# Kernel optimization log

Measured on AMD Instinct MI355X. Metric: run time of the kernel, lower is better.

Reference implementation:

```python
import jax, jax.numpy as jnp
import numpy as np

# Fixed production-scale sizes (equal-sized graphs so unbatch == reshape)
B, NQ, ND = 64, 32, 512     # graph pairs, query nodes/graph, data nodes/graph
DIN, D, K = 64, 128, 16     # GCN_in_size, GCN_out_size, NTN_k
DEG = 8                     # average degree


def _gcn(x, src, dst, W, b):
    """GCNConv with self loops + symmetric normalization (PyG semantics)."""
    N = x.shape[0]
    loop = jnp.arange(N)
    s = jnp.concatenate([src, loop])
    t = jnp.concatenate([dst, loop])
    deg = jax.ops.segment_sum(jnp.ones_like(t, x.dtype), t, num_segments=N)
    dinv = jnp.where(deg > 0, deg ** -0.5, 0.0)
    norm = (dinv[s] * dinv[t])[:, None]
    h = x @ W
    return jax.ops.segment_sum(h[s] * norm, t, num_segments=N) + b


def _three_gcn(x, ei, W1, b1, W2, b2, W3, b3):
    src, dst = ei[0], ei[1]
    h1 = jax.nn.relu(_gcn(x, src, dst, W1, b1))
    h2 = jax.nn.relu(_gcn(h1, src, dst, W2, b2))
    h3 = jax.nn.relu(_gcn(h2, src, dst, W3, b3))
    return h1, h2, h3


def _level(q, d, Wn, Vn, bn, cw, cb):
    """att_layer + NTN + elementwise mult + 1x1 conv + softmax over data nodes.
    q: [B,NQ,D], d: [B,ND,D] -> (softmaxed map [B,NQ,ND], raw map, he [B,K,NQ,ND])."""
    att = jax.nn.softmax(jnp.einsum('bqd,bnd->bqn', q, d) / jnp.sqrt(jnp.float32(D)), axis=-1)
    qW = jnp.einsum('bqd,kde->bkqe', q, Wn)           # [B,K,NQ,D]
    bil = jnp.einsum('bkqe,bne->bkqn', qW, d)          # [B,K,NQ,ND]
    lq = jnp.einsum('kd,bqd->bkq', Vn[:, :D], q)[:, :, :, None]
    ld = jnp.einsum('kd,bnd->bkn', Vn[:, D:], d)[:, :, None, :]
    he = jax.nn.sigmoid(bil + lq + ld + bn[None, :, None, None]) * att[:, None]
    e_raw = jnp.einsum('k,bkqn->bqn', cw, he) + cb     # 1x1 Conv2d(K->1)
    return jax.nn.softmax(e_raw, axis=-1), e_raw, he


def reference(x_d, edge_index_d, x_q, edge_index_q, batch_index_d, batch_index_q,
              W1, b1, W2, b2, W3, b3,
              Wn1, Vn1, bn1, cw1, cb1,
              Wn2, Vn2, bn2, cw2, cb2,
              Wn3, Vn3, bn3, cw3, cb3,
              w_end, b_end):
    d1, d2, d3 = _three_gcn(x_d, edge_index_d, W1, b1, W2, b2, W3, b3)
    q1, q2, q3 = _three_gcn(x_q, edge_index_q, W1, b1, W2, b2, W3, b3)
    # unbatch: batch indices are sorted with equal graph sizes -> reshape
    d1, d2, d3 = (t.reshape(B, ND, D) for t in (d1, d2, d3))
    q1, q2, q3 = (t.reshape(B, NQ, D) for t in (q1, q2, q3))
    e1, _, he1 = _level(q1, d1, Wn1, Vn1, bn1, cw1, cb1)
    _, e2raw, he2 = _level(q2, d2, Wn2, Vn2, bn2, cw2, cb2)
    e3, _, he3 = _level(q3, d3, Wn3, Vn3, bn3, cw3, cb3)
    # Faithful to source quirks: the zip unpack `e1,e2,e3,h1,h2,h1` rebinds h1 to
    # he_3 (he_1 is never used, he_3 appears twice) and end2 enters the concat
    # PRE-softmax (the softmaxed version was assigned to unused `nd2`).
    stack = jnp.concatenate([e1[:, None], e2raw[:, None], e3[:, None], he3, he2, he3], axis=1)
    out = jnp.einsum('c,bcqn->bqn', w_end, stack) + b_end  # con_end 1x1 conv + squeeze
    return jax.nn.softmax(out, axis=-1)                    # softmax over data nodes


def setup_inputs() -> dict:
    key = jax.random.key(0)
    k = jax.random.split(key, 40)
    n = jax.random.normal
    Nd, Nq = B * ND, B * NQ
    Ed, Eq = Nd * DEG, Nq * DEG
    gid_d = jnp.repeat(jnp.arange(B), ND * DEG)
    gid_q = jnp.repeat(jnp.arange(B), NQ * DEG)
    inp = {
        'x_d': n(k[0], (Nd, DIN), jnp.float32),
        'x_q': n(k[1], (Nq, DIN), jnp.float32),
        'edge_index_d': jnp.stack([jax.random.randint(k[2], (Ed,), 0, ND) + gid_d * ND,
                                   jax.random.randint(k[3], (Ed,), 0, ND) + gid_d * ND]),
        'edge_index_q': jnp.stack([jax.random.randint(k[4], (Eq,), 0, NQ) + gid_q * NQ,
                                   jax.random.randint(k[5], (Eq,), 0, NQ) + gid_q * NQ]),
        'batch_index_d': jnp.repeat(jnp.arange(B), ND),
        'batch_index_q': jnp.repeat(jnp.arange(B), NQ),
        'W1': n(k[6], (DIN, D), jnp.float32) / np.sqrt(DIN), 'b1': jnp.zeros((D,), jnp.float32),
        'W2': n(k[7], (D, D), jnp.float32) / np.sqrt(D), 'b2': jnp.zeros((D,), jnp.float32),
        'W3': n(k[8], (D, D), jnp.float32) / np.sqrt(D), 'b3': jnp.zeros((D,), jnp.float32),
    }
    for i, l in enumerate(('1', '2', '3')):
        inp['Wn' + l] = n(k[10 + 4 * i], (K, D, D), jnp.float32) / np.sqrt(D)
        inp['Vn' + l] = n(k[11 + 4 * i], (K, 2 * D), jnp.float32) / np.sqrt(2 * D)
        inp['bn' + l] = jnp.zeros((K,), jnp.float32)
        inp['cw' + l] = n(k[12 + 4 * i], (K,), jnp.float32) / np.sqrt(K)
        inp['cb' + l] = jnp.zeros((1,), jnp.float32)
    inp['w_end'] = n(k[25], (3 * K + 3,), jnp.float32) / np.sqrt(3 * K + 3)
    inp['b_end'] = jnp.zeros((1,), jnp.float32)
    return inp
```

## Files before the change

### kernel.cpp

```cpp
#include <hip/hip_runtime.h>
#include <math.h>

namespace {
constexpr int cB  = 64;
constexpr int cNQ = 32;
constexpr int cND = 512;
constexpr int cNd = cB * cND;
constexpr int cNq = cB * cNQ;
constexpr int cEd = cNd * 8;
constexpr int cEq = cNq * 8;
constexpr int LD_STRIDE = 516;
constexpr int NB_CVT = 2188, NB_T2BF = 808, NB_CNT = (cEd + cEq) / 256;
constexpr int NB_FILL = (cEd + cEq) / 256;
}

#define F4C(p) (*(const float4*)(p))
#define F4W(p) (*(float4*)(p))

typedef __attribute__((ext_vector_type(8))) __bf16 bf16x8;
typedef __attribute__((ext_vector_type(4))) float floatx4;

__device__ __forceinline__ ushort f2bf(float f) {
  union { float f; unsigned u; } v;
  v.f = f;
  unsigned u = v.u;
  return (ushort)((u + 0x7fffu + ((u >> 16) & 1u)) >> 16);
}
__device__ __forceinline__ float bf2f(ushort u) {
  union { unsigned u; float f; } v;
  v.u = ((unsigned)u) << 16;
  return v.f;
}
__device__ __forceinline__ float4 us4f4(ushort4 u) {
  return make_float4(bf2f(u.x), bf2f(u.y), bf2f(u.z), bf2f(u.w));
}
__device__ __forceinline__ ushort4 f4us4(float4 f) {
  ushort4 o;
  o.x = f2bf(f.x); o.y = f2bf(f.y); o.z = f2bf(f.z); o.w = f2bf(f.w);
  return o;
}
__device__ __forceinline__ float fexp2(float x) {
#if __has_builtin(__builtin_amdgcn_exp2f)
  return __builtin_amdgcn_exp2f(x);
#else
  return exp2f(x);
#endif
}
__device__ __forceinline__ float frcp(float x) {
#if __has_builtin(__builtin_amdgcn_rcpf)
  return __builtin_amdgcn_rcpf(x);
#else
  return 1.0f / x;
#endif
}
__device__ __forceinline__ float fsigmoid(float z) {
  return frcp(1.0f + fexp2(z * -1.4426950408889634f));
}
__device__ __forceinline__ float fexp(float x) { return fexp2(x * 1.4426950408889634f); }

__device__ __forceinline__ int swz_g(int j) { return (((j >> 3) & 7) << 3) | (j & 7); }

__global__ __launch_bounds__(256) void k_front(
    const float* __restrict__ xd, const float* __restrict__ xq,
    const float* __restrict__ v0, const float* __restrict__ v1,
    const float* __restrict__ v2, ushort* __restrict__ oxd, ushort* __restrict__ oxq,
    ushort* __restrict__ ov0, ushort* __restrict__ ov1, ushort* __restrict__ ov2,
    const float* __restrict__ W1, const float* __restrict__ W2,
    const float* __restrict__ W3, const float* __restrict__ Wn0,
    const float* __restrict__ Wn1, const float* __restrict__ Wn2,
    ushort* __restrict__ o1, ushort* __restrict__ o2, ushort* __restrict__ o3,
    ushort* __restrict__ on0, ushort* __restrict__ on1, ushort* __restrict__ on2,
    const int* __restrict__ dst_d, const int* __restrict__ dst_q,
    int* __restrict__ cnt_d, int* __restrict__ cnt_q) {
  __shared__ float tile[32][33];
  int blk = blockIdx.x, tid = threadIdx.x;
  if (blk < NB_CVT) {
    const float* src;
    ushort* dst;
    int i;
    if (blk < 2048) { src = xd; dst = oxd; i = blk * 256 + tid; }
    else if (blk < 2176) { src = xq; dst = oxq; i = (blk - 2048) * 256 + tid; }
    else if (blk < 2180) { src = v0; dst = ov0; i = (blk - 2176) * 256 + tid; }
    else if (blk < 2184) { src = v1; dst = ov1; i = (blk - 2180) * 256 + tid; }
    else { src = v2; dst = ov2; i = (blk - 2184) * 256 + tid; }
    *(ushort4*)(dst + (size_t)i * 4) = f4us4(F4C(src + (size_t)i * 4));
  } else if (blk < NB_CVT + NB_T2BF) {
    int b5 = blk - NB_CVT;
    const float* in;
    ushort* out;
    int R, C, bt, t;
    if (b5 < 8)        { in = W1;  out = o1;  R = 64;  C = 128; bt = 0; t = b5; }
    else if (b5 < 24)  { in = W2;  out = o2;  R = 128; C = 128; bt = 0; t = b5 - 8; }
    else if (b5 < 40)  { in = W3;  out = o3;  R = 128; C = 128; bt = 0; t = b5 - 24; }
    else if (b5 < 296) { in = Wn0; out = on0; R = 128; C = 128; bt = (b5 - 40) >> 4;  t = (b5 - 40) & 15; }
    else if (b5 < 552) { in = Wn1; out = on1; R = 128; C = 128; bt = (b5 - 296) >> 4; t = (b5 - 296) & 15; }
    else               { in = Wn2; out = on2; R = 128; C = 128; bt = (b5 - 552) >> 4; t = (b5 - 552) & 15; }
    int tilesC = C >> 5;
    int tr = t / tilesC, tc = t - tr * tilesC;
    int tx = tid & 31, ty = tid >> 5;
    const float* ib = in + (size_t)bt * R * C;
    ushort* ob = out + (size_t)bt * R * C;
#pragma unroll
    for (int i = 0; i < 4; ++i)
      tile[ty + i * 8][tx] = ib[(tr * 32 + ty + i * 8) * C + tc * 32 + tx];
    __syncthreads();
#pragma unroll
    for (int i = 0; i < 4; ++i)
      ob[(size_t)(tc * 32 + ty + i * 8) * R + tr * 32 + tx] = f2bf(tile[tx][ty + i * 8]);
  } else {
    int i = (blk - NB_CVT - NB_T2BF) * 256 + tid;
    if (i < cEd) atomicAdd(&cnt_d[dst_d[i]], 1);
    else atomicAdd(&cnt_q[dst_q[i - cEd]], 1);
  }
}

__global__ __launch_bounds__(512) void k_scan_dinv(
    const int* __restrict__ cnt_d, const int* __restrict__ cnt_q,
    int* __restrict__ rp_d, int* __restrict__ rp_q,
    float* __restrict__ dinv_d, float* __restrict__ dinv_q) {
  __shared__ int sh[512];
  int blk = blockIdx.x, tid = threadIdx.x;
  if (blk < 64) {
    int v = cnt_d[blk * 512 + tid];
    sh[tid] = v;
    __syncthreads();
    for (int off = 1; off < 512; off <<= 1) {
      int t = (tid >= off) ? sh[tid - off] : 0;
      __syncthreads();
      sh[tid] += t;
      __syncthreads();
    }
    rp_d[blk * 512 + tid] = blk * 4096 + sh[tid] - v;
  } else if (blk < 68) {
    int g = (blk - 64) * 16 + (tid >> 5);
    int lane32 = tid & 31;
    int v = cnt_q[g * 32 + lane32];
    int incl = v;
#pragma unroll
    for (int off = 1; off < 32; off <<= 1) {
      int t = __shfl_up(incl, off, 32);
      if (lane32 >= off) incl += t;
    }
    rp_q[g * 32 + lane32] = g * 256 + incl - v;
  } else {
    int i = (blk - 68) * 512 + tid;
    if (i < cNd) dinv_d[i] = 1.0f / sqrtf((float)(cnt_d[i] + 1));
    else dinv_q[i - cNd] = 1.0f / sqrtf((float)(cnt_q[i - cNd] + 1));
  }
}

__global__ __launch_bounds__(256) void k_fill_gemm1(
    const int* __restrict__ src_d, const int* __restrict__ dst_d,
    const int* __restrict__ src_q, const int* __restrict__ dst_q,
    const int* __restrict__ rp_d, const int* __restrict__ rp_q,
    int* __restrict__ cur_d, int* __restrict__ cur_q, int* __restrict__ col_d,
    int* __restrict__ col_q, const ushort* __restrict__ xdbf,
    const ushort* __restrict__ xqbf, const ushort* __restrict__ w1T,
    const float* __restrict__ dinv_d, const float* __restrict__ dinv_q,
    ushort* __restrict__ htmp) {
  int blk = blockIdx.x, tid = threadIdx.x;
  if (blk < NB_FILL) {
    int i = blk * 256 + tid;
    if (i < cEd) {
      int d = dst_d[i];
      int p = atomicAdd(&cur_d[d], 1);
      col_d[rp_d[d] + p] = src_d[i];
    } else {
      int j = i - cEd;
      int d = dst_q[j];
      int p = atomicAdd(&cur_q[d], 1);
      col_q[rp_q[d] + p] = src_q[j];
    }
    return;
  }
  int blk2 = blk - NB_FILL;
  int wave = tid >> 6, lane = tid & 63;
  int col = lane & 15, quad = lane >> 4;
  bool isQ = blk2 >= 512;
  int node0;
  if (isQ) node0 = (blk2 - 512) * 64;
  else node0 = swz_g(blk2) * 512 + (blk2 >> 6) * 64;
  int mloc = node0 + wave * 16;
  const ushort* X = isQ ? xqbf : xdbf;
  const float* dv = isQ ? dinv_q : dinv_d;
  size_t hbase = isQ ? (size_t)cNd : 0;
  floatx4 acc[8];
#pragma unroll
  for (int ct = 0; ct < 8; ++ct)
#pragma unroll
    for (int r = 0; r < 4; ++r) acc[ct][r] = 0.0f;
#pragma unroll
  for (int kc = 0; kc < 2; ++kc) {
    bf16x8 a = *(const bf16x8*)(X + (size_t)(mloc + col) * 64 + kc * 32 + quad * 8);
#pragma unroll
    for (int ct = 0; ct < 8; ++ct) {
      bf16x8 b = *(const bf16x8*)(w1T + (size_t)(ct * 16 + col) * 64 + kc * 32 + quad * 8);
      acc[ct] = __builtin_amdgcn_mfma_f32_16x16x32_bf16(a, b, acc[ct], 0, 0, 0);
    }
  }
  float sc[4];
#pragma unroll
  for (int r = 0; r < 4; ++r) sc[r] = dv[mloc + quad * 4 + r];
#pragma unroll
  for (int ct = 0; ct < 8; ++ct)
#pragma unroll
    for (int r = 0; r < 4; ++r)
      htmp[(hbase + mloc + quad * 4 + r) * 128 + ct * 16 + col] = f2bf(acc[ct][r] * sc[r]);
}

__global__ __launch_bounds__(256) void gmn_gather_merged(
    const ushort* __restrict__ htmp, const int* __restrict__ rp_d,
    const int* __restrict__ cnt_d, const int* __restrict__ col_d,
    const float* __restrict__ dinv_d, const int* __restrict__ rp_q,
    const int* __restrict__ cnt_q, const int* __restrict__ col_q,
    const float* __restrict__ dinv_q, const float* __restrict__ bias,
    ushort* __restrict__ dbf, ushort* __restrict__ qbf) {
  int blk = blockIdx.x, tid = threadIdx.x;
  bool isQ = blk >= 4096;
  int node;
  if (isQ) {
    int j = blk - 4096;
    node = swz_g(j) * 32 + (j >> 6) * 8 + (tid >> 5);
  } else {
    node = swz_g(blk) * 512 + (blk >> 6) * 8 + (tid >> 5);
  }
  int l = tid & 31;
  const ushort* hs = htmp + (isQ ? (size_t)cNd * 128 : 0);
  const int* rp = isQ ? rp_q : rp_d;
  const int* cnt = isQ ? cnt_q : cnt_d;
  const int* col = isQ ? col_q : col_d;
  const float* dinv = isQ ? dinv_q : dinv_d;
  ushort* outp = isQ ? qbf : dbf;
  int c = cnt[node], s0 = rp[node];
  float dt = dinv[node];
  float4 acc = us4f4(*(const ushort4*)(hs + (size_t)node * 128 + l * 4));
  int cm = c < 32 ? c : 32;
  for (int j0 = 0; j0 < cm; j0 += 8) {
    int ss[8];
    ushort4 v[8];
#pragma unroll
    for (int t = 0; t < 8; ++t) {
      int jj = j0 + t;
      ss[t] = (jj < cm) ? col[s0 + jj] : -1;
    }
#pragma unroll
    for (int t = 0; t < 8; ++t)
      if (ss[t] >= 0) v[t] = *(const ushort4*)(hs + (size_t)ss[t] * 128 + l * 4);
#pragma unroll
    for (int t = 0; t < 8; ++t) {
      if (ss[t] >= 0) {
        float4 f = us4f4(v[t]);
        acc.x += f.x; acc.y += f.y; acc.z += f.z; acc.w += f.w;
      }
    }
  }
  for (int j = 32; j < c; ++j) {
    int s = col[s0 + j];
    float4 f = us4f4(*(const ushort4*)(hs + (size_t)s * 128 + l * 4));
    acc.x += f.x; acc.y += f.y; acc.z += f.z; acc.w += f.w;
  }
  float4 bv = F4C(bias + l * 4);
  float4 r;
  r.x = fmaxf(acc.x * dt + bv.x, 0.0f);
  r.y = fmaxf(acc.y * dt + bv.y, 0.0f);
  r.z = fmaxf(acc.z * dt + bv.z, 0.0f);
  r.w = fmaxf(acc.w * dt + bv.w, 0.0f);
  *(ushort4*)(outp + (size_t)node * 128 + l * 4) = f4us4(r);
}

__global__ __launch_bounds__(256) void gmn_qw(const ushort* __restrict__ qbf,
                                              const ushort* __restrict__ wnT,
                                              ushort* __restrict__ qw) {
  int blk = blockIdx.x, tid = threadIdx.x;
  int wave = tid >> 6, lane = tid & 63;
  int col = lane & 15, quad = lane >> 4;
  int b = swz_g(blk), k = blk >> 6;
  int et0 = wave * 2;
  floatx4 acc[2][2];
#pragma unroll
  for (int qt = 0; qt < 2; ++qt)
#pragma unroll
    for (int ei = 0; ei < 2; ++ei)
#pragma unroll
      for (int r = 0; r < 4; ++r) acc[qt][ei][r] = 0.0f;
#pragma unroll
  for (int kc = 0; kc < 4; ++kc) {
    bf16x8 a0 = *(const bf16x8*)(qbf + (size_t)(b * 32 + col) * 128 + kc * 32 + quad * 8);
    bf16x8 a1 = *(const bf16x8*)(qbf + (size_t)(b * 32 + 16 + col) * 128 + kc * 32 + quad * 8);
#pragma unroll
    for (int ei = 0; ei < 2; ++ei) {
      bf16x8 bf = *(const bf16x8*)(wnT + (size_t)(k * 128 + (et0 + ei) * 16 + col) * 128 +
                                   kc * 32 + quad * 8);
      acc[0][ei] = __builtin_amdgcn_mfma_f32_16x16x32_bf16(a0, bf, acc[0][ei], 0, 0, 0);
      acc[1][ei] = __builtin_amdgcn_mfma_f32_16x16x32_bf16(a1, bf, acc[1][ei], 0, 0, 0);
    }
  }
#pragma unroll
  for (int qt = 0; qt < 2; ++qt)
#pragma unroll
    for (int ei = 0; ei < 2; ++ei)
#pragma unroll
      for (int r = 0; r < 4; ++r)
        qw[((size_t)(b * 16 + k) << 12) + (qt * 16 + quad * 4 + r) * 128 +
           (et0 + ei) * 16 + col] = f2bf(acc[qt][ei][r]);
}

__global__ __launch_bounds__(512, 2) void k_level_gemm(
    const ushort* __restrict__ qbf, const ushort* __restrict__ dbf,
    const ushort* __restrict__ qw, const ushort* __restrict__ vnbf,
    const float* __restrict__ bn, const float* __restrict__ cw,
    const float* __restrict__ w_end, const float* __restrict__ b_end,
    int o1, int o2, int hasF, int do_sm, int mode, int widx,
    float* __restrict__ accb, float* __restrict__ out,
    const ushort* __restrict__ gWT, const float* __restrict__ dinv_d,
    const float* __restrict__ dinv_q, ushort* __restrict__ htmp) {
  __shared__ float s_ld[16 * LD_STRIDE];
  __shared__ float s_lq[16 * 16];
  __shared__ float s_red[16 * 8];
  int tid = threadIdx.x;
  int wave = tid >> 6, lane = tid & 63;
  int col = lane & 15, quad = lane >> 4;

  if (blockIdx.x >= 128) {
    int gblk = blockIdx.x - 128;
    bool isQ = gblk >= 256;
    int node0;
    if (isQ) node0 = (gblk - 256) * 128;
    else node0 = swz_g(gblk) * 512 + (gblk >> 6) * 128;
    int mloc = node0 + wave * 16;
    const ushort* X = isQ ? qbf : dbf;
    const float* dv = isQ ? dinv_q : dinv_d;
    size_t hbase = isQ ? (size_t)cNd : 0;
    floatx4 acc[8];
#pragma unroll
    for (int ct = 0; ct < 8; ++ct)
#pragma unroll
      for (int r = 0; r < 4; ++r) acc[ct][r] = 0.0f;
#pragma unroll
    for (int kc = 0; kc < 4; ++kc) {
      bf16x8 a = *(const bf16x8*)(X + (size_t)(mloc + col) * 128 + kc * 32 + quad * 8);
#pragma unroll
      for (int ct = 0; ct < 8; ++ct) {
        bf16x8 b = *(const bf16x8*)(gWT + (size_t)(ct * 16 + col) * 128 + kc * 32 + quad * 8);
        acc[ct] = __builtin_amdgcn_mfma_f32_16x16x32_bf16(a, b, acc[ct], 0, 0, 0);
      }
    }
    float sc[4];
#pragma unroll
    for (int r = 0; r < 4; ++r) sc[r] = dv[mloc + quad * 4 + r];
#pragma unroll
    for (int ct = 0; ct < 8; ++ct)
#pragma unroll
      for (int r = 0; r < 4; ++r)
        htmp[(hbase + mloc + quad * 4 + r) * 128 + ct * 16 + col] = f2bf(acc[ct][r] * sc[r]);
    return;
  }

  int b = swz_g(blockIdx.x & 63);
  int qh = blockIdx.x >> 6;
  int n0 = wave * 64;

  bf16x8 bfr[4][4];
#pragma unroll
  for (int s = 0; s < 4; ++s)
#pragma unroll
    for (int kc = 0; kc < 4; ++kc)
      bfr[s][kc] = *(const bf16x8*)(dbf + ((size_t)(b * 512 + n0 + s * 16 + col) << 7) +
                                    kc * 32 + quad * 8);
  bf16x8 aq[4];
#pragma unroll
  for (int kc = 0; kc < 4; ++kc)
    aq[kc] = *(const bf16x8*)(qbf + (size_t)(b * 32 + qh * 16 + col) * 128 +
                              kc * 32 + quad * 8);

  floatx4 att[4];
#pragma unroll
  for (int s = 0; s < 4; ++s)
#pragma unroll
    for (int r = 0; r < 4; ++r) att[s][r] = 0.0f;
#pragma unroll
  for (int kc = 0; kc < 4; ++kc)
#pragma unroll
    for (int s = 0; s < 4; ++s)
      att[s] = __builtin_amdgcn_mfma_f32_16x16x32_bf16(aq[kc], bfr[s][kc], att[s], 0, 0, 0);
  const float sc = 0.088388347648318440550f;
#pragma unroll
  for (int s = 0; s < 4; ++s)
#pragma unroll
    for (int r = 0; r < 4; ++r) att[s][r] *= sc;

  {
    bf16x8 vn2[4];
#pragma unroll
    for (int kc = 0; kc < 4; ++kc)
      vn2[kc] = *(const bf16x8*)(vnbf + col * 256 + 128 + kc * 32 + quad * 8);
#pragma unroll
    for (int s = 0; s < 4; ++s) {
      floatx4 lda;
#pragma unroll
      for (int r = 0; r < 4; ++r) lda[r] = 0.0f;
#pragma unroll
      for (int kc = 0; kc < 4; ++kc)
        lda = __builtin_amdgcn_mfma_f32_16x16x32_bf16(bfr[s][kc], vn2[kc], lda, 0, 0, 0);
#pragma unroll
      for (int r = 0; r < 4; ++r)
        s_ld[col * LD_STRIDE + n0 + s * 16 + quad * 4 + r] = lda[r];
    }
  }
  if (wave == 0) {
    bf16x8 vn1[4];
#pragma unroll
    for (int kc = 0; kc < 4; ++kc)
      vn1[kc] = *(const bf16x8*)(vnbf + col * 256 + kc * 32 + quad * 8);
    floatx4 lqa;
#pragma unroll
    for (int r = 0; r < 4; ++r) lqa[r] = 0.0f;
#pragma unroll
    for (int kc = 0; kc < 4; ++kc)
      lqa = __builtin_amdgcn_mfma_f32_16x16x32_bf16(aq[kc], vn1[kc], lqa, 0, 0, 0);
#pragma unroll
    for (int r = 0; r < 4; ++r) s_lq[col * 16 + quad * 4 + r] = lqa[r];
  }
  __syncthreads();

  float red[4], M[4];
#pragma unroll
  for (int r = 0; r < 4; ++r) {
    float m = fmaxf(fmaxf(att[0][r], att[1][r]), fmaxf(att[2][r], att[3][r]));
#pragma unroll
    for (int o = 1; o < 16; o <<= 1) m = fmaxf(m, __shfl_xor(m, o, 64));
    red[r] = m;
  }
  if (col == 0)
#pragma unroll
    for (int r = 0; r < 4; ++r) s_red[(quad * 4 + r) * 8 + wave] = red[r];
  __syncthreads();
#pragma unroll
  for (int r = 0; r < 4; ++r) {
    float m = s_red[(quad * 4 + r) * 8];
#pragma unroll
    for (int w = 1; w < 8; ++w) m = fmaxf(m, s_red[(quad * 4 + r) * 8 + w]);
    M[r] = m;
  }
  __syncthreads();
#pragma unroll
  for (int s = 0; s < 4; ++s)
#pragma unroll
    for (int r = 0; r < 4; ++r) att[s][r] = fexp(att[s][r] - M[r]);
#pragma unroll
  for (int r = 0; r < 4; ++r) {
    float m = att[0][r] + att[1][r] + att[2][r] + att[3][r];
#pragma unroll
    for (int o = 1; o < 16; o <<= 1) m += __shfl_xor(m, o, 64);
    red[r] = m;
  }
  if (col == 0)
#pragma unroll
    for (int r = 0; r < 4; ++r) s_red[(quad * 4 + r) * 8 + wave] = red[r];
  __syncthreads();
#pragma unroll
  for (int r = 0; r < 4; ++r) {
    float m = s_red[(quad * 4 + r) * 8];
#pragma unroll
    for (int w = 1; w < 8; ++w) m += s_red[(quad * 4 + r) * 8 + w];
    M[r] = frcp(m);
  }
  __syncthreads();
#pragma unroll
  for (int s = 0; s < 4; ++s)
#pragma unroll
    for (int r = 0; r < 4; ++r) att[s][r] *= M[r];

  floatx4 eacc[4], facc[4];
#pragma unroll
  for (int s = 0; s < 4; ++s)
#pragma unroll
    for (int r = 0; r < 4; ++r) { eacc[s][r] = 0.0f; facc[s][r] = 0.0f; }

#pragma unroll 4
  for (int k = 0; k < 16; ++k) {
    const ushort* qk = qw + ((size_t)(b * 16 + k) << 12) + (qh * 16 + col) * 128 + quad * 8;
    bf16x8 a0 = *(const bf16x8*)(qk);
    bf16x8 a1 = *(const bf16x8*)(qk + 32);
    bf16x8 a2 = *(const bf16x8*)(qk + 64);
    bf16x8 a3 = *(const bf16x8*)(qk + 96);
    floatx4 bil[4];
#pragma unroll
    for (int s = 0; s < 4; ++s) {
#pragma unroll
      for (int r = 0; r < 4; ++r) bil[s][r] = 0.0f;
      bil[s] = __builtin_amdgcn_mfma_f32_16x16x32_bf16(a0, bfr[s][0], bil[s], 0, 0, 0);
      bil[s] = __builtin_amdgcn_mfma_f32_16x16x32_bf16(a1, bfr[s][1], bil[s], 0, 0, 0);
      bil[s] = __builtin_amdgcn_mfma_f32_16x16x32_bf16(a2, bfr[s][2], bil[s], 0, 0, 0);
      bil[s] = __builtin_amdgcn_mfma_f32_16x16x32_bf16(a3, bfr[s][3], bil[s], 0, 0, 0);
    }
    float bnk = bn[k], cwk = cw[k];
    float wkk = 0.0f;
    if (hasF) {
      wkk = w_end[o1 + k];
      if (o2 >= 0) wkk += w_end[o2 + k];
    }
    float lqv[4];
#pragma unroll
    for (int r = 0; r < 4; ++r) lqv[r] = s_lq[k * 16 + quad * 4 + r] + bnk;
#pragma unroll
    for (int s = 0; s < 4; ++s) {
      float ldv = s_ld[k * LD_STRIDE + n0 + s * 16 + col];
#pragma unroll
      for (int r = 0; r < 4; ++r) {
        float sg = fsigmoid(bil[s][r] + lqv[r] + ldv);
        eacc[s][r] += cwk * sg;
        facc[s][r] += wkk * sg;
      }
    }
  }

#pragma unroll
  for (int s = 0; s < 4; ++s)
#pragma unroll
    for (int r = 0; r < 4; ++r) {
      eacc[s][r] *= att[s][r];
      facc[s][r] *= att[s][r];
    }
  if (do_sm) {
#pragma unroll
    for (int r = 0; r < 4; ++r) {
      float m = fmaxf(fmaxf(eacc[0][r], eacc[1][r]), fmaxf(eacc[2][r], eacc[3][r]));
#pragma unroll
      for (int o = 1; o < 16; o <<= 1) m = fmaxf(m, __shfl_xor(m, o, 64));
      red[r] = m;
    }
    if (col == 0)
#pragma unroll
      for (int r = 0; r < 4; ++r) s_red[(quad * 4 + r) * 8 + wave] = red[r];
    __syncthreads();
#pragma unroll
    for (int r = 0; r < 4; ++r) {
      float m = s_red[(quad * 4 + r) * 8];
#pragma unroll
      for (int w = 1; w < 8; ++w) m = fmaxf(m, s_red[(quad * 4 + r) * 8 + w]);
      M[r] = m;
    }
    __syncthreads();
#pragma unroll
    for (int s = 0; s < 4; ++s)
#pragma unroll
      for (int r = 0; r < 4; ++r) eacc[s][r] = fexp(eacc[s][r] - M[r]);
#pragma unroll
    for (int r = 0; r < 4; ++r) {
      float m = eacc[0][r] + eacc[1][r] + eacc[2][r] + eacc[3][r];
#pragma unroll
      for (int o = 1; o < 16; o <<= 1) m += __shfl_xor(m, o, 64);
      red[r] = m;
    }
    if (col == 0)
#pragma unroll
      for (int r = 0; r < 4; ++r) s_red[(quad * 4 + r) * 8 + wave] = red[r];
    __syncthreads();
#pragma unroll
    for (int r = 0; r < 4; ++r) {
      float m = s_red[(quad * 4 + r) * 8];
#pragma unroll
      for (int w = 1; w < 8; ++w) m += s_red[(quad * 4 + r) * 8 + w];
      M[r] = frcp(m);
    }
    __syncthreads();
#pragma unroll
    for (int s = 0; s < 4; ++s)
#pragma unroll
      for (int r = 0; r < 4; ++r) eacc[s][r] *= M[r];
  }
  float w = w_end[widx];
#pragma unroll
  for (int s = 0; s < 4; ++s)
#pragma unroll
    for (int r = 0; r < 4; ++r) eacc[s][r] = w * eacc[s][r] + (hasF ? facc[s][r] : 0.0f);

  if (mode == 0) {
#pragma unroll
    for (int s = 0; s < 4; ++s)
#pragma unroll
      for (int r = 0; r < 4; ++r)
        accb[((size_t)(b * 32 + qh * 16 + quad * 4 + r) << 9) + n0 + s * 16 + col] =
            eacc[s][r];
  } else if (mode == 1) {
#pragma unroll
    for (int s = 0; s < 4; ++s)
#pragma unroll
      for (int r = 0; r < 4; ++r)
        accb[((size_t)(b * 32 + qh * 16 + quad * 4 + r) << 9) + n0 + s * 16 + col] +=
            eacc[s][r];
  } else {
    float be = b_end[0];
#pragma unroll
    for (int s = 0; s < 4; ++s)
#pragma unroll
      for (int r = 0; r < 4; ++r)
        eacc[s][r] += accb[((size_t)(b * 32 + qh * 16 + quad * 4 + r) << 9) +
                           n0 + s * 16 + col] + be;
#pragma unroll
    for (int r = 0; r < 4; ++r) {
      float m = fmaxf(fmaxf(eacc[0][r], eacc[1][r]), fmaxf(eacc[2][r], eacc[3][r]));
#pragma unroll
      for (int o = 1; o < 16; o <<= 1) m = fmaxf(m, __shfl_xor(m, o, 64));
      red[r] = m;
    }
    if (col == 0)
#pragma unroll
      for (int r = 0; r < 4; ++r) s_red[(quad * 4 + r) * 8 + wave] = red[r];
    __syncthreads();
#pragma unroll
    for (int r = 0; r < 4; ++r) {
      float m = s_red[(quad * 4 + r) * 8];
#pragma unroll
      for (int w2 = 1; w2 < 8; ++w2) m = fmaxf(m, s_red[(quad * 4 + r) * 8 + w2]);
      M[r] = m;
    }
    __syncthreads();
#pragma unroll
    for (int s = 0; s < 4; ++s)
#pragma unroll
      for (int r = 0; r < 4; ++r) eacc[s][r] = fexp(eacc[s][r] - M[r]);
#pragma unroll
    for (int r = 0; r < 4; ++r) {
      float m = eacc[0][r] + eacc[1][r] + eacc[2][r] + eacc[3][r];
#pragma unroll
      for (int o = 1; o < 16; o <<= 1) m += __shfl_xor(m, o, 64);
      red[r] = m;
    }
    if (col == 0)
#pragma unroll
      for (int r = 0; r < 4; ++r) s_red[(quad * 4 + r) * 8 + wave] = red[r];
    __syncthreads();
#pragma unroll
    for (int r = 0; r < 4; ++r) {
      float m = s_red[(quad * 4 + r) * 8];
#pragma unroll
      for (int w2 = 1; w2 < 8; ++w2) m += s_red[(quad * 4 + r) * 8 + w2];
      M[r] = frcp(m);
    }
#pragma unroll
    for (int s = 0; s < 4; ++s)
#pragma unroll
      for (int r = 0; r < 4; ++r)
        out[((size_t)(b * 32 + qh * 16 + quad * 4 + r) << 9) + n0 + s * 16 + col] =
            eacc[s][r] * M[r];
  }
}

extern "C" void kernel_launch(void* const* d_in, const int* in_sizes, int n_in,
                              void* d_out, int out_size, void* d_ws, size_t ws_size,
                              hipStream_t stream) {
  (void)in_sizes; (void)n_in; (void)out_size; (void)ws_size;
  const float* x_d = (const float*)d_in[0];
  const float* x_q = (const float*)d_in[1];
  const int* ei_d = (const int*)d_in[2];
  const int* ei_q = (const int*)d_in[3];
  const float* W1 = (const float*)d_in[6];
  const float* b1 = (const float*)d_in[7];
  const float* W2 = (const float*)d_in[8];
  const float* b2 = (const float*)d_in[9];
  const float* W3 = (const float*)d_in[10];
  const float* b3 = (const float*)d_in[11];
  const float* Wn[3] = {(const float*)d_in[12], (const float*)d_in[17], (const float*)d_in[22]};
  const float* Vn[3] = {(const float*)d_in[13], (const float*)d_in[18], (const float*)d_in[23]};
  const float* bn[3] = {(const float*)d_in[14], (const float*)d_in[19], (const float*)d_in[24]};
  const float* cw[3] = {(const float*)d_in[15], (const float*)d_in[20], (const float*)d_in[25]};
  const float* w_end = (const float*)d_in[27];
  const float* b_end = (const float*)d_in[28];
  float* out = (float*)d_out;

  char* wsp = (char*)d_ws;
  auto alloc = [&](size_t nbytes) {
    void* p = (void*)wsp;
    wsp += (nbytes + 255) & ~(size_t)255;
    return p;
  };
  int* cnt_d = (int*)alloc(cNd * 4);
  int* cnt_q = (int*)alloc(cNq * 4);
  int* cur_d = (int*)alloc(cNd * 4);
  int* cur_q = (int*)alloc(cNq * 4);
  float* dinv_d = (float*)alloc(cNd * 4);
  float* dinv_q = (float*)alloc(cNq * 4);
  int* rp_d = (int*)alloc(cNd * 4);
  int* rp_q = (int*)alloc(cNq * 4);
  int* col_d = (int*)alloc((size_t)cEd * 4);
  int* col_q = (int*)alloc((size_t)cEq * 4);
  ushort* xdbf = (ushort*)alloc((size_t)cNd * 64 * 2);
  ushort* xqbf = (ushort*)alloc((size_t)cNq * 64 * 2);
  ushort* w1T = (ushort*)alloc(128 * 64 * 2);
  ushort* w2T = (ushort*)alloc(128 * 128 * 2);
  ushort* w3T = (ushort*)alloc(128 * 128 * 2);
  ushort* wnT[3];
  for (int l = 0; l < 3; ++l) wnT[l] = (ushort*)alloc((size_t)16 * 128 * 128 * 2);
  ushort* vnbf[3];
  for (int l = 0; l < 3; ++l) vnbf[l] = (ushort*)alloc(16 * 256 * 2);
  ushort* htmp = (ushort*)alloc((size_t)(cNd + cNq) * 128 * 2);
  ushort* dbf = (ushort*)alloc((size_t)cNd * 128 * 2);
  ushort* qbf[3];
  for (int l = 0; l < 3; ++l) qbf[l] = (ushort*)alloc((size_t)cNq * 128 * 2);
  float* accb = (float*)alloc((size_t)cB * cNQ * cND * 4);
  ushort* qwbuf = (ushort*)alloc((size_t)cB * 16 * 32 * 128 * 2);

  const int* src_d = ei_d;
  const int* dst_d = ei_d + cEd;
  const int* src_q = ei_q;
  const int* dst_q = ei_q + cEq;

  hipMemsetAsync(cnt_d, 0, (size_t)2 * (cNd + cNq) * 4, stream);

  k_front<<<NB_CVT + NB_T2BF + NB_CNT, 256, 0, stream>>>(
      x_d, x_q, Vn[0], Vn[1], Vn[2], xdbf, xqbf, vnbf[0], vnbf[1], vnbf[2], W1, W2,
      W3, Wn[0], Wn[1], Wn[2], w1T, w2T, w3T, wnT[0], wnT[1], wnT[2], dst_d, dst_q,
      cnt_d, cnt_q);

  k_scan_dinv<<<136, 512, 0, stream>>>(cnt_d, cnt_q, rp_d, rp_q, dinv_d, dinv_q);

  k_fill_gemm1<<<NB_FILL + 544, 256, 0, stream>>>(
      src_d, dst_d, src_q, dst_q, rp_d, rp_q, cur_d, cur_q, col_d, col_q, xdbf, xqbf,
      w1T, dinv_d, dinv_q, htmp);

  const float* bias[3] = {b1, b2, b3};
  const ushort* nextWT[3] = {w2T, w3T, nullptr};
  const int o1s[3] = {0, 19, 3};
  const int o2s[3] = {-1, -1, 35};
  const int hasF[3] = {0, 1, 1};
  const int dosms[3] = {1, 0, 1};
  const int modes[3] = {0, 1, 2};

  for (int l = 0; l < 3; ++l) {
    gmn_gather_merged<<<(cNd + cNq) / 8, 256, 0, stream>>>(
        htmp, rp_d, cnt_d, col_d, dinv_d, rp_q, cnt_q, col_q, dinv_q, bias[l], dbf,
        qbf[l]);
    gmn_qw<<<1024, 256, 0, stream>>>(qbf[l], wnT[l], qwbuf);
    int grid = (l < 2) ? (128 + 272) : 128;
    k_level_gemm<<<grid, 512, 0, stream>>>(
        qbf[l], dbf, qwbuf, vnbf[l], bn[l], cw[l], w_end, b_end, o1s[l], o2s[l],
        hasF[l], dosms[l], modes[l], l, accb, out, nextWT[l], dinv_d, dinv_q, htmp);
  }
}
```

Baseline: 300.6 us.

## Restructure per-level GCN/NTN schedule to shift query-path work into neighboring kernels

Splits the per-level launches into two merged kernels. The first does the data-graph gather, then the query projection qW and the next-level query GEMM. The second does the level GEMM, the next data GEMM, and now also the query gather for the next level. Because the small query-path work runs alongside larger independent work, the schedule drops from nine launches to seven and shortens the serial dependency chain. In exchange, block-index dispatch gets more complex, and blocks of very different cost now share one grid, which can hurt load balance.

```diff
diff --git a/kernel.cpp b/kernel.cpp
--- a/kernel.cpp
+++ b/kernel.cpp
@@ -15,7 +15,6 @@
 }
 
 #define F4C(p) (*(const float4*)(p))
-#define F4W(p) (*(float4*)(p))
 
 typedef __attribute__((ext_vector_type(8))) __bf16 bf16x8;
 typedef __attribute__((ext_vector_type(4))) float floatx4;
@@ -59,6 +58,76 @@
 __device__ __forceinline__ float fexp(float x) { return fexp2(x * 1.4426950408889634f); }
 
 __device__ __forceinline__ int swz_g(int j) { return (((j >> 3) & 7) << 3) | (j & 7); }
+
+__device__ __forceinline__ void dev_gather_node(
+    int node, int l, const ushort* __restrict__ hs, const int* __restrict__ rp,
+    const int* __restrict__ cnt, const int* __restrict__ col,
+    const float* __restrict__ dinv, const float* __restrict__ bias,
+    ushort* __restrict__ outp) {
+  int c = cnt[node], s0 = rp[node];
+  float dt = dinv[node];
+  float4 acc = us4f4(*(const ushort4*)(hs + (size_t)node * 128 + l * 4));
+  int cm = c < 32 ? c : 32;
+  for (int j0 = 0; j0 < cm; j0 += 8) {
+    int ss[8];
+    ushort4 v[8];
+#pragma unroll
+    for (int t = 0; t < 8; ++t) {
+      int jj = j0 + t;
+      ss[t] = (jj < cm) ? col[s0 + jj] : -1;
+    }
+#pragma unroll
+    for (int t = 0; t < 8; ++t)
+      if (ss[t] >= 0) v[t] = *(const ushort4*)(hs + (size_t)ss[t] * 128 + l * 4);
+#pragma unroll
+    for (int t = 0; t < 8; ++t) {
+      if (ss[t] >= 0) {
+        float4 f = us4f4(v[t]);
+        acc.x += f.x; acc.y += f.y; acc.z += f.z; acc.w += f.w;
+      }
+    }
+  }
+  for (int j = 32; j < c; ++j) {
+    int s = col[s0 + j];
+    float4 f = us4f4(*(const ushort4*)(hs + (size_t)s * 128 + l * 4));
+    acc.x += f.x; acc.y += f.y; acc.z += f.z; acc.w += f.w;
+  }
+  float4 bv = F4C(bias + l * 4);
+  float4 r;
+  r.x = fmaxf(acc.x * dt + bv.x, 0.0f);
+  r.y = fmaxf(acc.y * dt + bv.y, 0.0f);
+  r.z = fmaxf(acc.z * dt + bv.z, 0.0f);
+  r.w = fmaxf(acc.w * dt + bv.w, 0.0f);
+  *(ushort4*)(outp + (size_t)node * 128 + l * 4) = f4us4(r);
+}
+
+__device__ __forceinline__ void dev_gemm128(
+    int mloc, const ushort* __restrict__ X, const ushort* __restrict__ WT,
+    const float* __restrict__ dv, ushort* __restrict__ H, size_t hbase,
+    int col, int quad) {
+  floatx4 acc[8];
+#pragma unroll
+  for (int ct = 0; ct < 8; ++ct)
+#pragma unroll
+    for (int r = 0; r < 4; ++r) acc[ct][r] = 0.0f;
+#pragma unroll
+  for (int kc = 0; kc < 4; ++kc) {
+    bf16x8 a = *(const bf16x8*)(X + (size_t)(mloc + col) * 128 + kc * 32 + quad * 8);
+#pragma unroll
+    for (int ct = 0; ct < 8; ++ct) {
+      bf16x8 b = *(const bf16x8*)(WT + (size_t)(ct * 16 + col) * 128 + kc * 32 + quad * 8);
+      acc[ct] = __builtin_amdgcn_mfma_f32_16x16x32_bf16(a, b, acc[ct], 0, 0, 0);
+    }
+  }
+  float sc[4];
+#pragma unroll
+  for (int r = 0; r < 4; ++r) sc[r] = dv[mloc + quad * 4 + r];
+#pragma unroll
+  for (int ct = 0; ct < 8; ++ct)
+#pragma unroll
+    for (int r = 0; r < 4; ++r)
+      H[(hbase + mloc + quad * 4 + r) * 128 + ct * 16 + col] = f2bf(acc[ct][r] * sc[r]);
+}
 
 __global__ __launch_bounds__(256) void k_front(
     const float* __restrict__ xd, const float* __restrict__ xq,
@@ -208,104 +277,74 @@
       htmp[(hbase + mloc + quad * 4 + r) * 128 + ct * 16 + col] = f2bf(acc[ct][r] * sc[r]);
 }
 
-__global__ __launch_bounds__(256) void gmn_gather_merged(
-    const ushort* __restrict__ htmp, const int* __restrict__ rp_d,
+__global__ __launch_bounds__(512, 4) void k_e1(
+    int aux, ushort* __restrict__ htmp, const int* __restrict__ rp_d,
     const int* __restrict__ cnt_d, const int* __restrict__ col_d,
     const float* __restrict__ dinv_d, const int* __restrict__ rp_q,
     const int* __restrict__ cnt_q, const int* __restrict__ col_q,
     const float* __restrict__ dinv_q, const float* __restrict__ bias,
-    ushort* __restrict__ dbf, ushort* __restrict__ qbf) {
-  int blk = blockIdx.x, tid = threadIdx.x;
-  bool isQ = blk >= 4096;
-  int node;
-  if (isQ) {
-    int j = blk - 4096;
-    node = swz_g(j) * 32 + (j >> 6) * 8 + (tid >> 5);
-  } else {
-    node = swz_g(blk) * 512 + (blk >> 6) * 8 + (tid >> 5);
-  }
-  int l = tid & 31;
-  const ushort* hs = htmp + (isQ ? (size_t)cNd * 128 : 0);
-  const int* rp = isQ ? rp_q : rp_d;
-  const int* cnt = isQ ? cnt_q : cnt_d;
-  const int* col = isQ ? col_q : col_d;
-  const float* dinv = isQ ? dinv_q : dinv_d;
-  ushort* outp = isQ ? qbf : dbf;
-  int c = cnt[node], s0 = rp[node];
-  float dt = dinv[node];
-  float4 acc = us4f4(*(const ushort4*)(hs + (size_t)node * 128 + l * 4));
-  int cm = c < 32 ? c : 32;
-  for (int j0 = 0; j0 < cm; j0 += 8) {
-    int ss[8];
-    ushort4 v[8];
-#pragma unroll
-    for (int t = 0; t < 8; ++t) {
-      int jj = j0 + t;
-      ss[t] = (jj < cm) ? col[s0 + jj] : -1;
-    }
-#pragma unroll
-    for (int t = 0; t < 8; ++t)
-      if (ss[t] >= 0) v[t] = *(const ushort4*)(hs + (size_t)ss[t] * 128 + l * 4);
-#pragma unroll
-    for (int t = 0; t < 8; ++t) {
-      if (ss[t] >= 0) {
-        float4 f = us4f4(v[t]);
-        acc.x += f.x; acc.y += f.y; acc.z += f.z; acc.w += f.w;
-      }
-    }
-  }
-  for (int j = 32; j < c; ++j) {
-    int s = col[s0 + j];
-    float4 f = us4f4(*(const ushort4*)(hs + (size_t)s * 128 + l * 4));
-    acc.x += f.x; acc.y += f.y; acc.z += f.z; acc.w += f.w;
-  }
-  float4 bv = F4C(bias + l * 4);
-  float4 r;
-  r.x = fmaxf(acc.x * dt + bv.x, 0.0f);
-  r.y = fmaxf(acc.y * dt + bv.y, 0.0f);
-  r.z = fmaxf(acc.z * dt + bv.z, 0.0f);
-  r.w = fmaxf(acc.w * dt + bv.w, 0.0f);
-  *(ushort4*)(outp + (size_t)node * 128 + l * 4) = f4us4(r);
-}
-
-__global__ __launch_bounds__(256) void gmn_qw(const ushort* __restrict__ qbf,
-                                              const ushort* __restrict__ wnT,
-                                              ushort* __restrict__ qw) {
+    ushort* __restrict__ dbf, ushort* __restrict__ qbf_out,
+    const ushort* __restrict__ qbf_lvl, const ushort* __restrict__ wnT,
+    ushort* __restrict__ qw, const ushort* __restrict__ gWT) {
   int blk = blockIdx.x, tid = threadIdx.x;
   int wave = tid >> 6, lane = tid & 63;
   int col = lane & 15, quad = lane >> 4;
-  int b = swz_g(blk), k = blk >> 6;
-  int et0 = wave * 2;
-  floatx4 acc[2][2];
-#pragma unroll
-  for (int qt = 0; qt < 2; ++qt)
-#pragma unroll
-    for (int ei = 0; ei < 2; ++ei)
-#pragma unroll
-      for (int r = 0; r < 4; ++r) acc[qt][ei][r] = 0.0f;
-#pragma unroll
-  for (int kc = 0; kc < 4; ++kc) {
-    bf16x8 a0 = *(const bf16x8*)(qbf + (size_t)(b * 32 + col) * 128 + kc * 32 + quad * 8);
-    bf16x8 a1 = *(const bf16x8*)(qbf + (size_t)(b * 32 + 16 + col) * 128 + kc * 32 + quad * 8);
-#pragma unroll
-    for (int ei = 0; ei < 2; ++ei) {
-      bf16x8 bf = *(const bf16x8*)(wnT + (size_t)(k * 128 + (et0 + ei) * 16 + col) * 128 +
-                                   kc * 32 + quad * 8);
-      acc[0][ei] = __builtin_amdgcn_mfma_f32_16x16x32_bf16(a0, bf, acc[0][ei], 0, 0, 0);
-      acc[1][ei] = __builtin_amdgcn_mfma_f32_16x16x32_bf16(a1, bf, acc[1][ei], 0, 0, 0);
-    }
-  }
-#pragma unroll
-  for (int qt = 0; qt < 2; ++qt)
-#pragma unroll
-    for (int ei = 0; ei < 2; ++ei)
-#pragma unroll
-      for (int r = 0; r < 4; ++r)
-        qw[((size_t)(b * 16 + k) << 12) + (qt * 16 + quad * 4 + r) * 128 +
-           (et0 + ei) * 16 + col] = f2bf(acc[qt][ei][r]);
-}
-
-__global__ __launch_bounds__(512, 2) void k_level_gemm(
+  int sec, sblk;
+  if (aux == 0) {
+    if (blk < 2048) { sec = 0; sblk = blk; } else { sec = 1; sblk = blk - 2048; }
+  } else if (aux == 1) {
+    if (blk < 2048) { sec = 0; sblk = blk; }
+    else if (blk < 2560) { sec = 2; sblk = blk - 2048; }
+    else { sec = 3; sblk = blk - 2560; }
+  } else {
+    if (blk < 512) { sec = 2; sblk = blk; } else { sec = 3; sblk = blk - 512; }
+  }
+
+  if (sec == 0) {
+    int node = swz_g(sblk & 63) * 512 + (sblk >> 6) * 16 + (tid >> 5);
+    dev_gather_node(node, tid & 31, htmp, rp_d, cnt_d, col_d, dinv_d, bias, dbf);
+  } else if (sec == 1) {
+    int node = swz_g(sblk & 63) * 32 + (sblk >> 6) * 16 + (tid >> 5);
+    dev_gather_node(node, tid & 31, htmp + (size_t)cNd * 128, rp_q, cnt_q, col_q,
+                    dinv_q, bias, qbf_out);
+  } else if (sec == 2) {
+    int b = swz_g(sblk & 63);
+    int k = (sblk >> 6) * 2 + (wave >> 2);
+    int et0 = (wave & 3) * 2;
+    floatx4 acc[2][2];
+#pragma unroll
+    for (int qt = 0; qt < 2; ++qt)
+#pragma unroll
+      for (int ei = 0; ei < 2; ++ei)
+#pragma unroll
+        for (int r = 0; r < 4; ++r) acc[qt][ei][r] = 0.0f;
+#pragma unroll
+    for (int kc = 0; kc < 4; ++kc) {
+      bf16x8 a0 = *(const bf16x8*)(qbf_lvl + (size_t)(b * 32 + col) * 128 + kc * 32 + quad * 8);
+      bf16x8 a1 = *(const bf16x8*)(qbf_lvl + (size_t)(b * 32 + 16 + col) * 128 + kc * 32 + quad * 8);
+#pragma unroll
+      for (int ei = 0; ei < 2; ++ei) {
+        bf16x8 bf = *(const bf16x8*)(wnT + (size_t)(k * 128 + (et0 + ei) * 16 + col) * 128 +
+                                     kc * 32 + quad * 8);
+        acc[0][ei] = __builtin_amdgcn_mfma_f32_16x16x32_bf16(a0, bf, acc[0][ei], 0, 0, 0);
+        acc[1][ei] = __builtin_amdgcn_mfma_f32_16x16x32_bf16(a1, bf, acc[1][ei], 0, 0, 0);
+      }
+    }
+#pragma unroll
+    for (int qt = 0; qt < 2; ++qt)
+#pragma unroll
+      for (int ei = 0; ei < 2; ++ei)
+#pragma unroll
+        for (int r = 0; r < 4; ++r)
+          qw[((size_t)(b * 16 + k) << 12) + (qt * 16 + quad * 4 + r) * 128 +
+             (et0 + ei) * 16 + col] = f2bf(acc[qt][ei][r]);
+  } else {
+    int mloc = sblk * 128 + wave * 16;
+    dev_gemm128(mloc, qbf_lvl, gWT, dinv_q, htmp, (size_t)cNd, col, quad);
+  }
+}
+
+__global__ __launch_bounds__(512, 2) void k_e2(
     const ushort* __restrict__ qbf, const ushort* __restrict__ dbf,
     const ushort* __restrict__ qw, const ushort* __restrict__ vnbf,
     const float* __restrict__ bn, const float* __restrict__ cw,
@@ -313,7 +352,10 @@
     int o1, int o2, int hasF, int do_sm, int mode, int widx,
     float* __restrict__ accb, float* __restrict__ out,
     const ushort* __restrict__ gWT, const float* __restrict__ dinv_d,
-    const float* __restrict__ dinv_q, ushort* __restrict__ htmp) {
+    const float* __restrict__ dinv_q, ushort* __restrict__ htmp,
+    const int* __restrict__ rp_q, const int* __restrict__ cnt_q,
+    const int* __restrict__ col_q, const float* __restrict__ bias_next,
+    ushort* __restrict__ qbf_next) {
   __shared__ float s_ld[16 * LD_STRIDE];
   __shared__ float s_lq[16 * 16];
   __shared__ float s_red[16 * 8];
@@ -321,38 +363,17 @@
   int wave = tid >> 6, lane = tid & 63;
   int col = lane & 15, quad = lane >> 4;
 
+  if (blockIdx.x >= 384) {
+    int j = blockIdx.x - 384;
+    int node = swz_g(j & 63) * 32 + (j >> 6) * 16 + (tid >> 5);
+    dev_gather_node(node, tid & 31, htmp + (size_t)cNd * 128, rp_q, cnt_q, col_q,
+                    dinv_q, bias_next, qbf_next);
+    return;
+  }
   if (blockIdx.x >= 128) {
-    int gblk = blockIdx.x - 128;
-    bool isQ = gblk >= 256;
-    int node0;
-    if (isQ) node0 = (gblk - 256) * 128;
-    else node0 = swz_g(gblk) * 512 + (gblk >> 6) * 128;
-    int mloc = node0 + wave * 16;
-    const ushort* X = isQ ? qbf : dbf;
-    const float* dv = isQ ? dinv_q : dinv_d;
-    size_t hbase = isQ ? (size_t)cNd : 0;
-    floatx4 acc[8];
-#pragma unroll
-    for (int ct = 0; ct < 8; ++ct)
-#pragma unroll
-      for (int r = 0; r < 4; ++r) acc[ct][r] = 0.0f;
-#pragma unroll
-    for (int kc = 0; kc < 4; ++kc) {
-      bf16x8 a = *(const bf16x8*)(X + (size_t)(mloc + col) * 128 + kc * 32 + quad * 8);
-#pragma unroll
-      for (int ct = 0; ct < 8; ++ct) {
-        bf16x8 b = *(const bf16x8*)(gWT + (size_t)(ct * 16 + col) * 128 + kc * 32 + quad * 8);
-        acc[ct] = __builtin_amdgcn_mfma_f32_16x16x32_bf16(a, b, acc[ct], 0, 0, 0);
-      }
-    }
-    float sc[4];
-#pragma unroll
-    for (int r = 0; r < 4; ++r) sc[r] = dv[mloc + quad * 4 + r];
-#pragma unroll
-    for (int ct = 0; ct < 8; ++ct)
-#pragma unroll
-      for (int r = 0; r < 4; ++r)
-        htmp[(hbase + mloc + quad * 4 + r) * 128 + ct * 16 + col] = f2bf(acc[ct][r] * sc[r]);
+    int g = blockIdx.x - 128;
+    int mloc = swz_g(g & 63) * 512 + (g >> 6) * 128 + wave * 16;
+    dev_gemm128(mloc, dbf, gWT, dinv_d, htmp, 0, col, quad);
     return;
   }
 
@@ -720,22 +741,31 @@
       src_d, dst_d, src_q, dst_q, rp_d, rp_q, cur_d, cur_q, col_d, col_q, xdbf, xqbf,
       w1T, dinv_d, dinv_q, htmp);
 
-  const float* bias[3] = {b1, b2, b3};
-  const ushort* nextWT[3] = {w2T, w3T, nullptr};
-  const int o1s[3] = {0, 19, 3};
-  const int o2s[3] = {-1, -1, 35};
-  const int hasF[3] = {0, 1, 1};
-  const int dosms[3] = {1, 0, 1};
-  const int modes[3] = {0, 1, 2};
-
-  for (int l = 0; l < 3; ++l) {
-    gmn_gather_merged<<<(cNd + cNq) / 8, 256, 0, stream>>>(
-        htmp, rp_d, cnt_d, col_d, dinv_d, rp_q, cnt_q, col_q, dinv_q, bias[l], dbf,
-        qbf[l]);
-    gmn_qw<<<1024, 256, 0, stream>>>(qbf[l], wnT[l], qwbuf);
-    int grid = (l < 2) ? (128 + 272) : 128;
-    k_level_gemm<<<grid, 512, 0, stream>>>(
-        qbf[l], dbf, qwbuf, vnbf[l], bn[l], cw[l], w_end, b_end, o1s[l], o2s[l],
-        hasF[l], dosms[l], modes[l], l, accb, out, nextWT[l], dinv_d, dinv_q, htmp);
-  }
-}
+  k_e1<<<2176, 512, 0, stream>>>(0, htmp, rp_d, cnt_d, col_d, dinv_d, rp_q, cnt_q,
+                                 col_q, dinv_q, b1, dbf, qbf[0], qbf[0], wnT[0],
+                                 qwbuf, w2T);
+
+  k_e1<<<528, 512, 0, stream>>>(2, htmp, rp_d, cnt_d, col_d, dinv_d, rp_q, cnt_q,
+                                col_q, dinv_q, b1, dbf, qbf[0], qbf[0], wnT[0],
+                                qwbuf, w2T);
+
+  k_e2<<<512, 512, 0, stream>>>(qbf[0], dbf, qwbuf, vnbf[0], bn[0], cw[0], w_end,
+                                b_end, 0, -1, 0, 1, 0, 0, accb, out, w2T, dinv_d,
+                                dinv_q, htmp, rp_q, cnt_q, col_q, b2, qbf[1]);
+
+  k_e1<<<2576, 512, 0, stream>>>(1, htmp, rp_d, cnt_d, col_d, dinv_d, rp_q, cnt_q,
+                                 col_q, dinv_q, b2, dbf, qbf[1], qbf[1], wnT[1],
+                                 qwbuf, w3T);
+
+  k_e2<<<512, 512, 0, stream>>>(qbf[1], dbf, qwbuf, vnbf[1], bn[1], cw[1], w_end,
+                                b_end, 19, -1, 1, 0, 1, 1, accb, out, w3T, dinv_d,
+                                dinv_q, htmp, rp_q, cnt_q, col_q, b3, qbf[2]);
+
+  k_e1<<<2560, 512, 0, stream>>>(1, htmp, rp_d, cnt_d, col_d, dinv_d, rp_q, cnt_q,
+                                 col_q, dinv_q, b3, dbf, qbf[2], qbf[2], wnT[2],
+                                 qwbuf, w3T);
+
+  k_e2<<<128, 512, 0, stream>>>(qbf[2], dbf, qwbuf, vnbf[2], bn[2], cw[2], w_end,
+                                b_end, 3, 35, 1, 1, 2, 2, accb, out, w3T, dinv_d,
+                                dinv_q, htmp, rp_q, cnt_q, col_q, b3, qbf[2]);
+}
```

After: 321.4 us. 1.07x slower.
